# Kernel tuning notes

Measured on AMD Instinct MI355X. Metric: run time of the kernel, lower is better.

The kernel has to match this reference:

```python
import jax, jax.numpy as jnp
import numpy as np

B, S, E = 64, 512, 1024
H = 16
D = E // H  # 64

def setup_inputs() -> dict:
    key = jax.random.key(0)
    ks = jax.random.split(key, 5)
    scale = 1.0 / np.sqrt(E)
    return {
        "hidden_states": jax.random.normal(ks[0], (B, S, E), dtype=jnp.float32),
        "Wq": jax.random.normal(ks[1], (E, E), dtype=jnp.float32) * scale,
        "Wk": jax.random.normal(ks[2], (E, E), dtype=jnp.float32) * scale,
        "Wv": jax.random.normal(ks[3], (E, E), dtype=jnp.float32) * scale,
        "Wo": jax.random.normal(ks[4], (E, E), dtype=jnp.float32) * scale,
        "bo": jnp.zeros((E,), dtype=jnp.float32),
    }

def reference(hidden_states, Wq, Wk, Wv, Wo, bo):
    b, s, e = hidden_states.shape
    # projections (bias-free), split heads -> [B, H, S, D]
    def split(x):
        return x.reshape(b, s, H, D).transpose(0, 2, 1, 3)
    q = split(hidden_states @ Wq)
    k = split(hidden_states @ Wk)
    v = split(hidden_states @ Wv)
    # NOTE: original module applies NO 1/sqrt(d) scaling
    scores = jnp.einsum('bhqd,bhkd->bhqk', q.astype(jnp.float32), k.astype(jnp.float32))
    causal = jnp.tril(jnp.ones((s, s), dtype=bool))  # [S, S]
    mask_value = jnp.finfo(scores.dtype).min
    scores = jnp.where(causal[None, None, :, :], scores, mask_value)
    attn = jax.nn.softmax(scores, axis=-1).astype(v.dtype)
    out = jnp.einsum('bhqk,bhkd->bhqd', attn, v)  # [B, H, S, D]
    out = out.transpose(0, 2, 1, 3).reshape(b, s, e)  # merge heads
    out = out @ Wo + bo
    return out
```

## Files before the change

kernel.cpp:

```cpp
#include <hip/hip_runtime.h>
#include <hip/hip_bf16.h>
#include <cstdint>
#include <cstddef>

#define B_ 64
#define S_ 512
#define E_ 1024
#define H_ 16
#define D_ 64

typedef __attribute__((ext_vector_type(8))) short s8v;
typedef __attribute__((ext_vector_type(4))) float f4v;

__device__ __forceinline__ ushort f2bf(float f) {
  uint32_t u = __builtin_bit_cast(uint32_t, f);
  u += 0x7fffu + ((u >> 16) & 1u);
  return (ushort)(u >> 16);
}

__device__ __forceinline__ void async_cp16(const void* g, void* l) {
  __builtin_amdgcn_global_load_lds(
      (const __attribute__((address_space(1))) unsigned int*)g,
      (__attribute__((address_space(3))) unsigned int*)(uintptr_t)l,
      16, 0, 0);
}

__global__ __launch_bounds__(256) void convertx(const float* __restrict__ X,
                                                ushort* __restrict__ Y) {
  size_t i = ((size_t)blockIdx.x * 256 + threadIdx.x) * 4;
  float4 v = *(const float4*)(X + i);
  uint2 p;
  p.x = (uint32_t)f2bf(v.x) | ((uint32_t)f2bf(v.y) << 16);
  p.y = (uint32_t)f2bf(v.z) | ((uint32_t)f2bf(v.w) << 16);
  *(uint2*)(Y + i) = p;
}

__global__ __launch_bounds__(256) void transpose_w(const float* __restrict__ W,
                                                   ushort* __restrict__ Wt) {
  __shared__ ushort T[32][33];
  int x = threadIdx.x & 31, y = threadIdx.x >> 5;
  int c0 = blockIdx.x * 32;
  int r0 = blockIdx.y * 32;
#pragma unroll
  for (int i = 0; i < 4; i++) {
    int r = y + i * 8;
    T[x][r] = f2bf(W[(size_t)(r0 + r) * E_ + c0 + x]);
  }
  __syncthreads();
#pragma unroll
  for (int i = 0; i < 4; i++) {
    int r = y + i * 8;
    Wt[(size_t)(c0 + r) * E_ + r0 + x] = T[r][x];
  }
}

__device__ __forceinline__ void gemm256_core(const ushort* __restrict__ A,
                                             const ushort* __restrict__ Bt,
                                             int m0, int n0, ushort* smem,
                                             f4v acc[8][4]) {
  const int tid = threadIdx.x;
  const int wave = tid >> 6, lane = tid & 63;
  const int wm = wave >> 2, wn = wave & 3;
  const int lrow = lane & 15, quad = lane >> 4;
  const int swl = lrow & 7;
  const int ch0 = (quad ^ swl) * 8;
  const int ch1 = ((4 + quad) ^ swl) * 8;
  const int arow = (wm * 128 + lrow) * 64;
  const int brow = (wn * 64 + lrow) * 64;
  const int rr = tid >> 3;
  const int sq = ((tid & 7) ^ (rr & 7)) * 8;
  const ushort* Ab = A + (size_t)m0 * E_;
  const ushort* Bb = Bt + (size_t)n0 * E_;

#define SA_(buf) (smem + (buf) * 16384)
#define SB_(buf) (smem + 32768 + (buf) * 16384)

  auto STG = [&](const ushort* g, ushort* l) {
#pragma unroll
    for (int i = 0; i < 4; i++)
      async_cp16(g + (size_t)(rr + i * 64) * E_ + sq, l + i * 4096 + tid * 8);
  };

#pragma unroll
  for (int i = 0; i < 8; i++)
#pragma unroll
    for (int j = 0; j < 4; j++) acc[i][j] = (f4v){0.f, 0.f, 0.f, 0.f};

  STG(Ab + 0, SA_(0));
  STG(Bb + 0, SB_(0));
  STG(Ab + 64, SA_(1));
  STG(Bb + 64, SB_(1));
  asm volatile("s_waitcnt vmcnt(8)" ::: "memory");
  __builtin_amdgcn_s_barrier();

  for (int t = 0; t < 16; ++t) {
    const int buf = t & 1;
    const ushort* As = SA_(buf);
    const ushort* Bs = SB_(buf);
    s8v a[4], b[4];

#pragma unroll
    for (int i = 0; i < 4; i++) a[i] = *(const s8v*)(As + arow + i * 1024 + ch0);
#pragma unroll
    for (int n = 0; n < 4; n++) b[n] = *(const s8v*)(Bs + brow + n * 1024 + ch0);
    __builtin_amdgcn_s_barrier();
    __builtin_amdgcn_s_setprio(1);
#pragma unroll
    for (int i = 0; i < 4; i++)
#pragma unroll
      for (int n = 0; n < 4; n++)
        acc[i][n] = __builtin_amdgcn_mfma_f32_16x16x32_bf16(a[i], b[n], acc[i][n], 0, 0, 0);
    __builtin_amdgcn_s_setprio(0);
    __builtin_amdgcn_s_barrier();

#pragma unroll
    for (int i = 0; i < 4; i++) a[i] = *(const s8v*)(As + arow + (4 + i) * 1024 + ch0);
    __builtin_amdgcn_s_barrier();
    __builtin_amdgcn_s_setprio(1);
#pragma unroll
    for (int i = 0; i < 4; i++)
#pragma unroll
      for (int n = 0; n < 4; n++)
        acc[4 + i][n] = __builtin_amdgcn_mfma_f32_16x16x32_bf16(a[i], b[n], acc[4 + i][n], 0, 0, 0);
    __builtin_amdgcn_s_setprio(0);
    __builtin_amdgcn_s_barrier();

#pragma unroll
    for (int i = 0; i < 4; i++) a[i] = *(const s8v*)(As + arow + i * 1024 + ch1);
#pragma unroll
    for (int n = 0; n < 4; n++) b[n] = *(const s8v*)(Bs + brow + n * 1024 + ch1);
    __builtin_amdgcn_s_barrier();
    __builtin_amdgcn_s_setprio(1);
#pragma unroll
    for (int i = 0; i < 4; i++)
#pragma unroll
      for (int n = 0; n < 4; n++)
        acc[i][n] = __builtin_amdgcn_mfma_f32_16x16x32_bf16(a[i], b[n], acc[i][n], 0, 0, 0);
    __builtin_amdgcn_s_setprio(0);
    __builtin_amdgcn_s_barrier();

#pragma unroll
    for (int i = 0; i < 4; i++) a[i] = *(const s8v*)(As + arow + (4 + i) * 1024 + ch1);
    __builtin_amdgcn_s_barrier();
    __builtin_amdgcn_s_setprio(1);
#pragma unroll
    for (int i = 0; i < 4; i++)
#pragma unroll
      for (int n = 0; n < 4; n++)
        acc[4 + i][n] = __builtin_amdgcn_mfma_f32_16x16x32_bf16(a[i], b[n], acc[4 + i][n], 0, 0, 0);
    __builtin_amdgcn_s_setprio(0);
    if (t < 14) {
      STG(Ab + (size_t)(t + 2) * 64, SA_(buf));
      STG(Bb + (size_t)(t + 2) * 64, SB_(buf));
      asm volatile("s_waitcnt vmcnt(8)" ::: "memory");
    } else if (t == 14) {
      asm volatile("s_waitcnt vmcnt(0)" ::: "memory");
    }
    __builtin_amdgcn_s_barrier();
  }
#undef SA_
#undef SB_
}

__global__ __launch_bounds__(512, 2) void gemm_qkv(
    const ushort* __restrict__ A, const ushort* __restrict__ Bt,
    ushort* __restrict__ Qo, ushort* __restrict__ Ko, ushort* __restrict__ Vt) {
  __shared__ __align__(16) ushort smem[65536];
  const int orig = blockIdx.x;
  const int swz = (orig & 7) * 192 + (orig >> 3);
  const int ntile = swz % 12, mtile = swz / 12;
  const int n0 = ntile * 256, m0 = mtile * 256;

  f4v acc[8][4];
  gemm256_core(A, Bt, m0, n0, smem, acc);

  const int tid = threadIdx.x;
  const int wave = tid >> 6, lane = tid & 63;
  const int wm = wave >> 2, wn = wave & 3;
  const int lrow = lane & 15, quad = lane >> 4;
  const int proj = n0 >> 10;
  const int np0 = n0 & 1023;
  const int hb = np0 >> 6;
  const int bb = m0 >> 9, s0 = m0 & 511;

  if (proj < 2) {
    ushort* C = proj == 0 ? Qo : Ko;
#pragma unroll
    for (int h = 0; h < 2; h++) {
#pragma unroll
      for (int mf = 0; mf < 4; mf++)
#pragma unroll
        for (int n = 0; n < 4; n++)
#pragma unroll
          for (int r = 0; r < 4; r++)
            smem[(wm * 64 + mf * 16 + quad * 4 + r) * 264 + wn * 64 + n * 16 + lrow] =
                f2bf(acc[h * 4 + mf][n][r]);
      __syncthreads();
#pragma unroll
      for (int j = 0; j < 8; j++) {
        int chunk = j * 512 + tid;
        int pr = chunk >> 5, cc = chunk & 31;
        int s = s0 + (pr >> 6) * 128 + h * 64 + (pr & 63);
        int hd = hb + (cc >> 3);
        size_t off = (((size_t)bb * H_ + hd) * S_ + s) * D_ + (cc & 7) * 8;
        *(uint4*)&C[off] = *(const uint4*)&smem[pr * 264 + cc * 8];
      }
      if (h == 0) __syncthreads();
    }
  } else {
#pragma unroll
    for (int w = 0; w < 2; w++) {
      if (wm == w) {
#pragma unroll
        for (int m = 0; m < 8; m++)
#pragma unroll
          for (int n = 0; n < 4; n++) {
            ushort4 pk;
            pk.x = f2bf(acc[m][n][0]);
            pk.y = f2bf(acc[m][n][1]);
            pk.z = f2bf(acc[m][n][2]);
            pk.w = f2bf(acc[m][n][3]);
            *(ushort4*)&smem[(wn * 64 + n * 16 + lrow) * 136 + m * 16 + quad * 4] = pk;
          }
      }
      __syncthreads();
#pragma unroll
      for (int j = 0; j < 8; j++) {
        int chunk = j * 512 + tid;
        int dr = chunk >> 4, cc = chunk & 15;
        int hd = hb + (dr >> 6), d = dr & 63;
        size_t off = (((size_t)bb * H_ + hd) * D_ + d) * S_ + s0 + w * 128 + cc * 8;
        *(uint4*)&Vt[off] = *(const uint4*)&smem[dr * 136 + cc * 8];
      }
      if (w == 0) __syncthreads();
    }
  }
}

__global__ __launch_bounds__(512, 2) void gemm_o(
    const ushort* __restrict__ A, const ushort* __restrict__ Bt,
    float* __restrict__ C, const float* __restrict__ bias) {
  __shared__ __align__(16) ushort smem[65536];
  const int orig = blockIdx.x;
  const int swz = (orig & 7) * 64 + (orig >> 3);
  const int ntile = swz & 3, mtile = swz >> 2;
  const int n0 = ntile * 256, m0 = mtile * 256;

  f4v acc[8][4];
  gemm256_core(A, Bt, m0, n0, smem, acc);

  const int tid = threadIdx.x;
  const int wave = tid >> 6, lane = tid & 63;
  const int wm = wave >> 2, wn = wave & 3;
  const int lrow = lane & 15, quad = lane >> 4;
#pragma unroll
  for (int n = 0; n < 4; n++) {
    int col = n0 + wn * 64 + n * 16 + lrow;
    float bv = bias[col];
#pragma unroll
    for (int m = 0; m < 8; m++) {
      int row = m0 + wm * 128 + m * 16 + quad * 4;
#pragma unroll
      for (int r = 0; r < 4; r++)
        C[(size_t)(row + r) * E_ + col] = acc[m][n][r] + bv;
    }
  }
}

__global__ __launch_bounds__(256, 3) void attn_kernel(
    const ushort* __restrict__ Qg, const ushort* __restrict__ Kg,
    const ushort* __restrict__ Vtg, ushort* __restrict__ AO) {
  __shared__ __align__(16) ushort Ks[2][64 * 64];
  __shared__ __align__(16) ushort Vts[2][64 * 64];
  __shared__ __align__(16) ushort Ps[4][32 * 72];

  const int qp = blockIdx.x;
  const int bh = blockIdx.y;
  const int b = bh >> 4, h = bh & 15;
  const int tid = threadIdx.x, wave = tid >> 6, lane = tid & 63;
  const int lrow = lane & 15, quad = lane >> 4;
  const int swl = lrow & 7;
  const size_t base = (size_t)bh * (S_ * D_);
  const int qB0 = qp * 64 + wave * 16;
  const int qB1 = (7 - qp) * 64 + wave * 16;
  const int kd0 = qp, kd1 = 7 - qp;
  const int NT = kd1 + 1;

  s8v qf[2][2];
#pragma unroll
  for (int kk = 0; kk < 2; kk++) {
    qf[0][kk] = *(const s8v*)(Qg + base + (size_t)(qB0 + lrow) * 64 + kk * 32 + quad * 8);
    qf[1][kk] = *(const s8v*)(Qg + base + (size_t)(qB1 + lrow) * 64 + kk * 32 + quad * 8);
  }

  f4v o[2][4];
#pragma unroll
  for (int mi = 0; mi < 2; mi++)
#pragma unroll
    for (int di = 0; di < 4; di++) o[mi][di] = (f4v){0.f, 0.f, 0.f, 0.f};
  float mr[2] = {-INFINITY, -INFINITY};
  float lr[2] = {0.f, 0.f};

  ushort* pw = &Ps[wave][0];

  auto STAGE = [&](int kt, int bf) {
#pragma unroll
    for (int i = 0; i < 2; i++) {
      int c = i * 256 + tid;
      int r = c >> 3, cc = c & 7;
      int sc = cc ^ (r & 7);
      async_cp16(Kg + base + (size_t)(kt * 64 + r) * 64 + sc * 8, (void*)&Ks[bf][c * 8]);
    }
#pragma unroll
    for (int i = 0; i < 2; i++) {
      int c = i * 256 + tid;
      int d = c >> 3, cc = c & 7;
      int sc = cc ^ (d & 7);
      async_cp16(Vtg + base + (size_t)d * S_ + kt * 64 + sc * 8, (void*)&Vts[bf][c * 8]);
    }
  };

  STAGE(0, 0);
  __syncthreads();

  int buf = 0;
  for (int kt = 0; kt < NT; kt++) {
    if (kt + 1 < NT) STAGE(kt + 1, buf ^ 1);
    const bool act0 = (kt <= kd0);
    const ushort* Kb = &Ks[buf][0];
    const ushort* Vb = &Vts[buf][0];

    f4v st[2][4];
#pragma unroll
    for (int mi = 0; mi < 2; mi++)
#pragma unroll
      for (int ni = 0; ni < 4; ni++) st[mi][ni] = (f4v){0.f, 0.f, 0.f, 0.f};
    __builtin_amdgcn_s_setprio(1);
#pragma unroll
    for (int kk = 0; kk < 2; kk++) {
      const int ch = (kk * 4 + quad) ^ swl;
#pragma unroll
      for (int ni = 0; ni < 4; ni++) {
        s8v kf = *(const s8v*)&Kb[(ni * 16 + lrow) * 64 + ch * 8];
        st[1][ni] = __builtin_amdgcn_mfma_f32_16x16x32_bf16(kf, qf[1][kk], st[1][ni], 0, 0, 0);
        if (act0)
          st[0][ni] = __builtin_amdgcn_mfma_f32_16x16x32_bf16(kf, qf[0][kk], st[0][ni], 0, 0, 0);
      }
    }
    __builtin_amdgcn_s_setprio(0);

    float alr[2][4];
#pragma unroll
    for (int mi = 0; mi < 2; mi++) {
      if (mi == 0 && !act0) continue;
      const int qB = mi ? qB1 : qB0;
      if (kt == (mi ? kd1 : kd0)) {
        int qrow = qB + lrow;
#pragma unroll
        for (int ni = 0; ni < 4; ni++) {
          int kc0 = kt * 64 + ni * 16 + quad * 4;
#pragma unroll
          for (int r = 0; r < 4; r++)
            if (kc0 + r > qrow) st[mi][ni][r] = -INFINITY;
        }
      }
      float bm = st[mi][0][0];
#pragma unroll
      for (int ni = 0; ni < 4; ni++)
#pragma unroll
        for (int r = 0; r < 4; r++) bm = fmaxf(bm, st[mi][ni][r]);
      bm = fmaxf(bm, __shfl_xor(bm, 16));
      bm = fmaxf(bm, __shfl_xor(bm, 32));
      float mn = fmaxf(mr[mi], bm);
      float al = __expf(mr[mi] - mn);
      mr[mi] = mn;
      float bs = 0.f;
#pragma unroll
      for (int ni = 0; ni < 4; ni++) {
        float p0 = __expf(st[mi][ni][0] - mn);
        float p1 = __expf(st[mi][ni][1] - mn);
        float p2 = __expf(st[mi][ni][2] - mn);
        float p3 = __expf(st[mi][ni][3] - mn);
        bs += (p0 + p1) + (p2 + p3);
        ushort4 pk = {f2bf(p0), f2bf(p1), f2bf(p2), f2bf(p3)};
        *(ushort4*)&pw[(mi * 16 + lrow) * 72 + ni * 16 + quad * 4] = pk;
      }
      bs += __shfl_xor(bs, 16);
      bs += __shfl_xor(bs, 32);
      lr[mi] = lr[mi] * al + bs;
#pragma unroll
      for (int r = 0; r < 4; r++) alr[mi][r] = __shfl(al, (lane & 48) + quad * 4 + r);
#pragma unroll
      for (int di = 0; di < 4; di++)
#pragma unroll
        for (int r = 0; r < 4; r++) o[mi][di][r] *= alr[mi][r];
    }

    __builtin_amdgcn_s_setprio(1);
#pragma unroll
    for (int kk = 0; kk < 2; kk++) {
      const int ch = (kk * 4 + quad) ^ swl;
      s8v pf1 = *(const s8v*)&pw[(16 + lrow) * 72 + kk * 32 + quad * 8];
      if (act0) {
        s8v pf0 = *(const s8v*)&pw[lrow * 72 + kk * 32 + quad * 8];
#pragma unroll
        for (int di = 0; di < 4; di++) {
          s8v vf = *(const s8v*)&Vb[(di * 16 + lrow) * 64 + ch * 8];
          o[1][di] = __builtin_amdgcn_mfma_f32_16x16x32_bf16(pf1, vf, o[1][di], 0, 0, 0);
          o[0][di] = __builtin_amdgcn_mfma_f32_16x16x32_bf16(pf0, vf, o[0][di], 0, 0, 0);
        }
      } else {
#pragma unroll
        for (int di = 0; di < 4; di++) {
          s8v vf = *(const s8v*)&Vb[(di * 16 + lrow) * 64 + ch * 8];
          o[1][di] = __builtin_amdgcn_mfma_f32_16x16x32_bf16(pf1, vf, o[1][di], 0, 0, 0);
        }
      }
    }
    __builtin_amdgcn_s_setprio(0);

    __syncthreads();
    buf ^= 1;
  }

  float inv[2][4];
#pragma unroll
  for (int mi = 0; mi < 2; mi++)
#pragma unroll
    for (int r = 0; r < 4; r++)
      inv[mi][r] = 1.0f / __shfl(lr[mi], (lane & 48) + quad * 4 + r);

#pragma unroll
  for (int mi = 0; mi < 2; mi++)
#pragma unroll
    for (int di = 0; di < 4; di++)
#pragma unroll
      for (int r = 0; r < 4; r++)
        pw[(mi * 16 + quad * 4 + r) * 72 + di * 16 + lrow] = f2bf(o[mi][di][r] * inv[mi][r]);

#pragma unroll
  for (int i = 0; i < 4; i++) {
    int c = i * 64 + lane;
    int row = c >> 3, cc = c & 7;
    uint4 val = *(const uint4*)&pw[row * 72 + cc * 8];
    int q = ((row >> 4) ? qB1 : qB0) + (row & 15);
    size_t off = ((size_t)b * S_ + q) * E_ + h * 64 + cc * 8;
    *(uint4*)&AO[off] = val;
  }
}

extern "C" void kernel_launch(void* const* d_in, const int* in_sizes, int n_in,
                              void* d_out, int out_size, void* d_ws, size_t ws_size,
                              hipStream_t stream) {
  const float* X = (const float*)d_in[0];
  const float* Wq = (const float*)d_in[1];
  const float* Wk = (const float*)d_in[2];
  const float* Wv = (const float*)d_in[3];
  const float* Wo = (const float*)d_in[4];
  const float* bo = (const float*)d_in[5];
  float* out = (float*)d_out;

  char* ws = (char*)d_ws;
  ushort* Xb = (ushort*)(ws);
  ushort* Wqkvt = (ushort*)(ws + 67108864);
  ushort* Wot = (ushort*)(ws + 73400320);
  ushort* Qb = (ushort*)(ws + 75497472);
  ushort* Kb = (ushort*)(ws + 142606336);
  ushort* Vtb = (ushort*)(ws + 209715200);
  ushort* AO = Xb;

  convertx<<<32768, 256, 0, stream>>>(X, Xb);
  transpose_w<<<dim3(32, 32), 256, 0, stream>>>(Wq, Wqkvt);
  transpose_w<<<dim3(32, 32), 256, 0, stream>>>(Wk, Wqkvt + 1024 * 1024);
  transpose_w<<<dim3(32, 32), 256, 0, stream>>>(Wv, Wqkvt + 2 * 1024 * 1024);
  transpose_w<<<dim3(32, 32), 256, 0, stream>>>(Wo, Wot);

  gemm_qkv<<<1536, 512, 0, stream>>>(Xb, Wqkvt, Qb, Kb, Vtb);

  attn_kernel<<<dim3(4, 1024), 256, 0, stream>>>(Qb, Kb, Vtb, AO);

  gemm_o<<<512, 512, 0, stream>>>(AO, Wot, out, bo);
}
```

Before: 640.1 us.

## Split GEMM K-tiles into half-tiles and interleave async loads with MFMA phases

The shared-memory layout of the 256x256 GEMM core changes so each 64-wide K tile is stored as two 32-wide halves, each with its own XOR swizzle. Global-to-LDS async copies are issued one half at a time between the MFMA phases instead of in one burst at the end of each iteration, with the vmcnt waits adjusted to match. The aim is to spread memory traffic across the iteration and hide load latency behind compute. The cost is more complex wait-count bookkeeping and a different LDS bank-conflict pattern.

```diff
diff --git a/kernel.cpp b/kernel.cpp
--- a/kernel.cpp
+++ b/kernel.cpp
@@ -62,23 +62,22 @@
   const int wave = tid >> 6, lane = tid & 63;
   const int wm = wave >> 2, wn = wave & 3;
   const int lrow = lane & 15, quad = lane >> 4;
-  const int swl = lrow & 7;
-  const int ch0 = (quad ^ swl) * 8;
-  const int ch1 = ((4 + quad) ^ swl) * 8;
-  const int arow = (wm * 128 + lrow) * 64;
-  const int brow = (wn * 64 + lrow) * 64;
-  const int rr = tid >> 3;
-  const int sq = ((tid & 7) ^ (rr & 7)) * 8;
+  const int slot8 = (quad ^ ((lrow >> 1) & 3)) * 8;
+  const int arow = (wm * 128 + lrow) * 32 + slot8;
+  const int brow = (wn * 64 + lrow) * 32 + slot8;
+  const int srow = tid >> 2;
+  const int c8 = ((tid & 3) ^ ((tid >> 3) & 3)) * 8;
   const ushort* Ab = A + (size_t)m0 * E_;
   const ushort* Bb = Bt + (size_t)n0 * E_;
 
-#define SA_(buf) (smem + (buf) * 16384)
-#define SB_(buf) (smem + 32768 + (buf) * 16384)
-
-  auto STG = [&](const ushort* g, ushort* l) {
-#pragma unroll
-    for (int i = 0; i < 4; i++)
-      async_cp16(g + (size_t)(rr + i * 64) * E_ + sq, l + i * 4096 + tid * 8);
+#define AH_(buf, kh) (smem + ((buf) * 2 + (kh)) * 8192)
+#define BH_(buf, kh) (smem + 32768 + ((buf) * 2 + (kh)) * 8192)
+
+  auto STGH = [&](const ushort* g, int kh, ushort* l) {
+#pragma unroll
+    for (int i = 0; i < 2; i++)
+      async_cp16(g + (size_t)(srow + i * 128) * E_ + kh * 32 + c8,
+                 l + i * 4096 + tid * 8);
   };
 
 #pragma unroll
@@ -86,23 +85,28 @@
 #pragma unroll
     for (int j = 0; j < 4; j++) acc[i][j] = (f4v){0.f, 0.f, 0.f, 0.f};
 
-  STG(Ab + 0, SA_(0));
-  STG(Bb + 0, SB_(0));
-  STG(Ab + 64, SA_(1));
-  STG(Bb + 64, SB_(1));
+  STGH(Ab, 0, AH_(0, 0));
+  STGH(Bb, 0, BH_(0, 0));
+  STGH(Ab, 1, AH_(0, 1));
+  STGH(Bb, 1, BH_(0, 1));
+  STGH(Ab + 64, 0, AH_(1, 0));
+  STGH(Bb + 64, 0, BH_(1, 0));
   asm volatile("s_waitcnt vmcnt(8)" ::: "memory");
   __builtin_amdgcn_s_barrier();
 
   for (int t = 0; t < 16; ++t) {
     const int buf = t & 1;
-    const ushort* As = SA_(buf);
-    const ushort* Bs = SB_(buf);
+    const ushort* A0s = AH_(buf, 0);
+    const ushort* A1s = AH_(buf, 1);
+    const ushort* B0s = BH_(buf, 0);
+    const ushort* B1s = BH_(buf, 1);
     s8v a[4], b[4];
 
 #pragma unroll
-    for (int i = 0; i < 4; i++) a[i] = *(const s8v*)(As + arow + i * 1024 + ch0);
-#pragma unroll
-    for (int n = 0; n < 4; n++) b[n] = *(const s8v*)(Bs + brow + n * 1024 + ch0);
+    for (int i = 0; i < 4; i++) a[i] = *(const s8v*)(A0s + arow + i * 512);
+#pragma unroll
+    for (int n = 0; n < 4; n++) b[n] = *(const s8v*)(B0s + brow + n * 512);
+    if (t < 15) STGH(Ab + (size_t)(t + 1) * 64, 1, AH_(buf ^ 1, 1));
     __builtin_amdgcn_s_barrier();
     __builtin_amdgcn_s_setprio(1);
 #pragma unroll
@@ -114,7 +118,8 @@
     __builtin_amdgcn_s_barrier();
 
 #pragma unroll
-    for (int i = 0; i < 4; i++) a[i] = *(const s8v*)(As + arow + (4 + i) * 1024 + ch0);
+    for (int i = 0; i < 4; i++) a[i] = *(const s8v*)(A0s + arow + (4 + i) * 512);
+    if (t < 15) STGH(Bb + (size_t)(t + 1) * 64, 1, BH_(buf ^ 1, 1));
     __builtin_amdgcn_s_barrier();
     __builtin_amdgcn_s_setprio(1);
 #pragma unroll
@@ -123,12 +128,18 @@
       for (int n = 0; n < 4; n++)
         acc[4 + i][n] = __builtin_amdgcn_mfma_f32_16x16x32_bf16(a[i], b[n], acc[4 + i][n], 0, 0, 0);
     __builtin_amdgcn_s_setprio(0);
-    __builtin_amdgcn_s_barrier();
-
-#pragma unroll
-    for (int i = 0; i < 4; i++) a[i] = *(const s8v*)(As + arow + i * 1024 + ch1);
-#pragma unroll
-    for (int n = 0; n < 4; n++) b[n] = *(const s8v*)(Bs + brow + n * 1024 + ch1);
+    if (t < 15) {
+      asm volatile("s_waitcnt vmcnt(8)" ::: "memory");
+    } else {
+      asm volatile("s_waitcnt vmcnt(0)" ::: "memory");
+    }
+    __builtin_amdgcn_s_barrier();
+
+#pragma unroll
+    for (int i = 0; i < 4; i++) a[i] = *(const s8v*)(A1s + arow + i * 512);
+#pragma unroll
+    for (int n = 0; n < 4; n++) b[n] = *(const s8v*)(B1s + brow + n * 512);
+    if (t < 14) STGH(Ab + (size_t)(t + 2) * 64, 0, AH_(buf, 0));
     __builtin_amdgcn_s_barrier();
     __builtin_amdgcn_s_setprio(1);
 #pragma unroll
@@ -140,7 +151,8 @@
     __builtin_amdgcn_s_barrier();
 
 #pragma unroll
-    for (int i = 0; i < 4; i++) a[i] = *(const s8v*)(As + arow + (4 + i) * 1024 + ch1);
+    for (int i = 0; i < 4; i++) a[i] = *(const s8v*)(A1s + arow + (4 + i) * 512);
+    if (t < 14) STGH(Bb + (size_t)(t + 2) * 64, 0, BH_(buf, 0));
     __builtin_amdgcn_s_barrier();
     __builtin_amdgcn_s_setprio(1);
 #pragma unroll
@@ -150,16 +162,14 @@
         acc[4 + i][n] = __builtin_amdgcn_mfma_f32_16x16x32_bf16(a[i], b[n], acc[4 + i][n], 0, 0, 0);
     __builtin_amdgcn_s_setprio(0);
     if (t < 14) {
-      STG(Ab + (size_t)(t + 2) * 64, SA_(buf));
-      STG(Bb + (size_t)(t + 2) * 64, SB_(buf));
       asm volatile("s_waitcnt vmcnt(8)" ::: "memory");
     } else if (t == 14) {
-      asm volatile("s_waitcnt vmcnt(0)" ::: "memory");
-    }
-    __builtin_amdgcn_s_barrier();
-  }
-#undef SA_
-#undef SB_
+      asm volatile("s_waitcnt vmcnt(4)" ::: "memory");
+    }
+    __builtin_amdgcn_s_barrier();
+  }
+#undef AH_
+#undef BH_
 }
 
 __global__ __launch_bounds__(512, 2) void gemm_qkv(
```

Result: faster. 614.1 us (-4.1%).
